# Kernel optimization log

Measured on AMD Instinct MI355X. Metric: run time of the kernel, lower is better.

Reference implementation:

```python
import jax, jax.numpy as jnp
import numpy as np

D_MODEL, N_HEADS, RANK = 1024, 16, 32
HEAD_DIM = D_MODEL // N_HEADS
B, S = 4, 2048


def setup_inputs() -> dict:
    key = jax.random.key(0)
    ks = jax.random.split(key, 8)
    inp = {
        "x": jax.random.normal(ks[0], (B, S, D_MODEL), dtype=jnp.float32),
        "mask": jnp.ones((B, S), dtype=jnp.int32),
        "qkv_u": jax.random.normal(ks[1], (D_MODEL, RANK), jnp.float32) / D_MODEL ** 0.5,
        "qkv_v": jax.random.normal(ks[2], (RANK, 3 * D_MODEL), jnp.float32) / RANK ** 0.5,
        "qkv_b": jnp.zeros((3 * D_MODEL,), jnp.float32),
        "u_attn": jax.random.normal(ks[3], (N_HEADS, HEAD_DIM, RANK), jnp.float32) / HEAD_DIM ** 0.5,
        "v_attn": jax.random.normal(ks[4], (N_HEADS, RANK, HEAD_DIM), jnp.float32) / RANK ** 0.5,
        "out_u": jax.random.normal(ks[5], (D_MODEL, RANK), jnp.float32) / D_MODEL ** 0.5,
        "out_v": jax.random.normal(ks[6], (RANK, D_MODEL), jnp.float32) / RANK ** 0.5,
        "out_b": jnp.zeros((D_MODEL,), jnp.float32),
    }
    return inp


def reference(x, mask, qkv_u, qkv_v, qkv_b, u_attn, v_attn, out_u, out_v, out_b):
    bs, seq_len, d_model = x.shape
    n_heads, head_dim, rank = u_attn.shape
    scale = 1.0 / jnp.sqrt(jnp.float32(rank))

    # Low-rank QKV projection: [B,S,3D]
    qkv = (x @ qkv_u) @ qkv_v + qkv_b
    q, k, v = jnp.split(qkv, 3, axis=-1)

    def to_heads(t):  # [B,S,D] -> [B,H,S,hd]
        return t.reshape(bs, seq_len, n_heads, head_dim).transpose(0, 2, 1, 3)

    q, k, v = to_heads(q), to_heads(k), to_heads(v)

    # Rank-projected Q/K: [B,H,S,r]
    q_low = jnp.einsum("bhsd,hdr->bhsr", q, u_attn)
    k_low = jnp.einsum("bhtd,hdr->bhtr", k, u_attn)
    scores = jnp.einsum("bhsr,bhtr->bhst", q_low, k_low) * scale

    # mask: [B,S] keys; masked_fill where mask == 0
    scores = jnp.where(mask[:, None, None, :] == 0, jnp.float32(-jnp.inf), scores)
    attn = jax.nn.softmax(scores, axis=-1)  # dropout is identity in eval

    v_low = jnp.einsum("bhtd,hdr->bhtr", v, u_attn)
    context_low = jnp.einsum("bhst,bhtr->bhsr", attn, v_low)
    context = jnp.einsum("bhsr,hrd->bhsd", context_low, v_attn)
    context = context.transpose(0, 2, 1, 3).reshape(bs, seq_len, d_model)

    return (context @ out_u) @ out_v + out_b
```

## Files before the change

### kernel.cpp

```cpp
#include <hip/hip_runtime.h>
#include <hip/hip_bf16.h>

typedef unsigned int u32;
typedef unsigned short u16;
typedef __attribute__((ext_vector_type(8))) __bf16 bf16x8;
typedef __attribute__((ext_vector_type(16))) float f32x16;
typedef __attribute__((ext_vector_type(2))) unsigned int u32x2;

#define QSCALE 0.25505418f
#define MFMA __builtin_amdgcn_mfma_f32_32x32x16_bf16

static __device__ __forceinline__ u16 f2b(float f) {
  __hip_bfloat16 h = __float2bfloat16(f);
  return *reinterpret_cast<u16*>(&h);
}
static __device__ __forceinline__ u32 cvtpk(float lo, float hi) {
  u32 r;
  asm("v_cvt_pk_bf16_f32 %0, %1, %2" : "=v"(r) : "v"(lo), "v"(hi));
  return r;
}

static __device__ __forceinline__ float xhalf_sum(float v) {
#if __has_builtin(__builtin_amdgcn_permlane32_swap)
  u32 a = __float_as_uint(v);
  u32x2 r = __builtin_amdgcn_permlane32_swap(a, a, false, false);
  return __uint_as_float(r[0]) + __uint_as_float(r[1]);
#else
  return v + __shfl_xor(v, 32);
#endif
}

static __device__ __forceinline__ int tau(int p) {
  int g = p >> 2;
  int gk = (g & 4) | ((g & 1) << 1) | ((g >> 1) & 1);
  return (gk << 2) | (p & 3);
}

__global__ __launch_bounds__(256) void k_prep(const float* __restrict__ qkv_v,
                                              const float* __restrict__ qkv_b,
                                              const float* __restrict__ u_attn,
                                              const float* __restrict__ v_attn,
                                              const float* __restrict__ out_u,
                                              const float* __restrict__ qkv_u,
                                              const float* __restrict__ out_v,
                                              u16* __restrict__ WQT, u16* __restrict__ WKT,
                                              u16* __restrict__ WVT, float* __restrict__ BQKV,
                                              u16* __restrict__ WOT, u16* __restrict__ UT,
                                              u16* __restrict__ OVT) {
  int blk = blockIdx.x;
  int tid = threadIdx.x;
  if (blk < 16) {
    int h = blk;
    int r = tid & 31, g = tid >> 5;
    for (int rp = g; rp < 32; rp += 8) {
      float aq = 0.f, ak = 0.f, av = 0.f;
      for (int d = 0; d < 64; ++d) {
        float u = u_attn[(h * 64 + d) * 32 + r];
        aq += qkv_v[rp * 3072 + h * 64 + d] * u;
        ak += qkv_v[rp * 3072 + 1024 + h * 64 + d] * u;
        av += qkv_v[rp * 3072 + 2048 + h * 64 + d] * u;
      }
      WQT[(h * 32 + r) * 32 + rp] = f2b(aq);
      WKT[(h * 32 + r) * 32 + rp] = f2b(ak);
      WVT[(h * 32 + r) * 32 + rp] = f2b(av);
    }
    for (int rr = g; rr < 32; rr += 8) {
      float a = 0.f;
      for (int d = 0; d < 64; ++d)
        a += v_attn[(h * 32 + rr) * 64 + d] * out_u[(h * 64 + d) * 32 + r];
      WOT[r * 512 + h * 32 + rr] = f2b(a);
    }
    if (tid < 32) {
      float aq = 0.f, ak = 0.f, av = 0.f;
      for (int d = 0; d < 64; ++d) {
        float u = u_attn[(h * 64 + d) * 32 + r];
        aq += qkv_b[h * 64 + d] * u;
        ak += qkv_b[1024 + h * 64 + d] * u;
        av += qkv_b[2048 + h * 64 + d] * u;
      }
      BQKV[h * 32 + r] = aq;
      BQKV[512 + h * 32 + r] = ak;
      BQKV[1024 + h * 32 + r] = av;
    }
  } else if (blk < 24) {
    int kb = (blk - 16) * 128;
    for (int i = tid; i < 4096; i += 256) {
      int r = i >> 7, kl = i & 127;
      UT[r * 1024 + kb + kl] = f2b(qkv_u[(kb + kl) * 32 + r]);
    }
  } else {
    int db = (blk - 24) * 128;
    for (int i = tid; i < 4096; i += 256) {
      int dl = i >> 5, r = i & 31;
      OVT[(db + dl) * 32 + r] = f2b(out_v[r * 1024 + db + dl]);
    }
  }
}

__global__ __launch_bounds__(512) void k_proj(const float* __restrict__ x,
                                              const u16* __restrict__ UT,
                                              u16* __restrict__ T) {
  __shared__ float red[8][32][33];
  int tid = threadIdx.x;
  int w = tid >> 6, l = tid & 63, lo = l & 31, hi = l >> 5;
  int m0 = blockIdx.x * 32;
  const float* xp = x + (size_t)(m0 + lo) * 1024 + w * 128 + hi * 8;
  const u16* up = UT + lo * 1024 + w * 128 + hi * 8;
  f32x16 acc = {};
  for (int s = 0; s < 8; ++s) {
    float4 x0 = *(const float4*)(xp);
    float4 x1 = *(const float4*)(xp + 4);
    xp += 16;
    union { bf16x8 v; u32 u[4]; } af;
    af.u[0] = cvtpk(x0.x, x0.y);
    af.u[1] = cvtpk(x0.z, x0.w);
    af.u[2] = cvtpk(x1.x, x1.y);
    af.u[3] = cvtpk(x1.z, x1.w);
    bf16x8 bf = *(const bf16x8*)(up);
    up += 16;
    acc = MFMA(af.v, bf, acc, 0, 0, 0);
  }
#pragma unroll
  for (int i = 0; i < 16; ++i)
    red[w][(i & 3) + 8 * (i >> 2) + 4 * hi][lo] = acc[i];
  __syncthreads();
  int m = tid >> 4, c = (tid & 15) * 2;
  float v0 = 0.f, v1 = 0.f;
#pragma unroll
  for (int ww = 0; ww < 8; ++ww) {
    v0 += red[ww][m][c + 0];
    v1 += red[ww][m][c + 1];
  }
  *(u32*)(T + (size_t)(m0 + m) * 32 + c) = cvtpk(v0, v1);
}

__global__ __launch_bounds__(256) void k_lowproj(const u16* __restrict__ T,
                                                 const u16* __restrict__ WQT,
                                                 const u16* __restrict__ WKT,
                                                 const u16* __restrict__ WVT,
                                                 const float* __restrict__ BQKV,
                                                 u16* __restrict__ QL, u16* __restrict__ KF,
                                                 u16* __restrict__ VF) {
  __shared__ float vtf[32][132];
  int tid = threadIdx.x;
  int w = tid >> 6, l = tid & 63, lo = l & 31, hi = l >> 5;
  int blk = blockIdx.x;
  int bh = blk >> 4, sb = (blk & 15) * 128;
  int b = bh >> 4, h = bh & 15;
  int s0 = sb + w * 32;

  const u16* wq = WQT + (h * 32 + lo) * 32 + hi * 8;
  const u16* wk = WKT + (h * 32 + lo) * 32 + hi * 8;
  const u16* wv = WVT + (h * 32 + lo) * 32 + hi * 8;
  bf16x8 aq0 = *(const bf16x8*)(wq), aq1 = *(const bf16x8*)(wq + 16);
  bf16x8 ak0 = *(const bf16x8*)(wk), ak1 = *(const bf16x8*)(wk + 16);
  bf16x8 av0 = *(const bf16x8*)(wv), av1 = *(const bf16x8*)(wv + 16);

  const u16* tp = T + (size_t)(b * 2048 + s0 + lo) * 32 + hi * 8;
  bf16x8 tb0 = *(const bf16x8*)(tp), tb1 = *(const bf16x8*)(tp + 16);

  f32x16 cq = {}, ck = {}, cv = {};
  cq = MFMA(aq0, tb0, cq, 0, 0, 0);
  cq = MFMA(aq1, tb1, cq, 0, 0, 0);
  ck = MFMA(ak0, tb0, ck, 0, 0, 0);
  ck = MFMA(ak1, tb1, ck, 0, 0, 0);
  cv = MFMA(av0, tb0, cv, 0, 0, 0);
  cv = MFMA(av1, tb1, cv, 0, 0, 0);

  size_t sg = (size_t)bh * 2048 + s0 + lo;
  size_t tbase = (size_t)bh * 65536 + (size_t)((sb >> 5) + w) * 1024;
  int slp = w * 32 + tau(lo);
#pragma unroll
  for (int g2 = 0; g2 < 4; ++g2) {
    float4 bq4 = *(const float4*)(BQKV + h * 32 + g2 * 8 + 4 * hi);
    float4 bk4 = *(const float4*)(BQKV + 512 + h * 32 + g2 * 8 + 4 * hi);
    float4 bv4 = *(const float4*)(BQKV + 1024 + h * 32 + g2 * 8 + 4 * hi);
    float q0 = (cq[4 * g2 + 0] + bq4.x) * QSCALE;
    float q1 = (cq[4 * g2 + 1] + bq4.y) * QSCALE;
    float q2 = (cq[4 * g2 + 2] + bq4.z) * QSCALE;
    float q3 = (cq[4 * g2 + 3] + bq4.w) * QSCALE;
    uint2 qo; qo.x = cvtpk(q0, q1); qo.y = cvtpk(q2, q3);
    *(uint2*)(QL + sg * 32 + g2 * 8 + 4 * hi) = qo;
    uint2 ko;
    ko.x = cvtpk(ck[4 * g2 + 0] + bk4.x, ck[4 * g2 + 1] + bk4.y);
    ko.y = cvtpk(ck[4 * g2 + 2] + bk4.z, ck[4 * g2 + 3] + bk4.w);
    *(uint2*)(KF + tbase + (g2 >> 1) * 512 + (g2 & 1) * 256 + lo * 8 + 4 * hi) = ko;
    int rbase = g2 * 8 + 4 * hi;
    vtf[rbase + 0][slp] = cv[4 * g2 + 0] + bv4.x;
    vtf[rbase + 1][slp] = cv[4 * g2 + 1] + bv4.y;
    vtf[rbase + 2][slp] = cv[4 * g2 + 2] + bv4.z;
    vtf[rbase + 3][slp] = cv[4 * g2 + 3] + bv4.w;
  }
  __syncthreads();
  for (int u = tid; u < 512; u += 256) {
    int r = u >> 4, su = (u & 15) * 8;
    const float* src = &vtf[r][su];
    uint4 o;
    o.x = cvtpk(src[0], src[1]);
    o.y = cvtpk(src[2], src[3]);
    o.z = cvtpk(src[4], src[5]);
    o.w = cvtpk(src[6], src[7]);
    int c = su & 31, tloc = su >> 5;
    *(uint4*)(VF + (size_t)bh * 65536 + (size_t)((sb >> 5) + tloc) * 1024 +
              (c >> 4) * 512 + ((c >> 3) & 1) * 256 + r * 8) = o;
  }
}

__global__ __launch_bounds__(256) void k_attn(const u16* __restrict__ QL,
                                              const u16* __restrict__ KF,
                                              const u16* __restrict__ VF,
                                              const int* __restrict__ mask,
                                              u16* __restrict__ CTX) {
  __shared__ float pacc[2][64][17];
  __shared__ float pl[2][64];
  __shared__ u32 cls[64][17];
  int tid = threadIdx.x;
  int wave = tid >> 6, l = tid & 63, lo = l & 31, hi = l >> 5;
  int blk = blockIdx.x;
  int xcd = blk & 7, slot = blk >> 3;
  int bh = xcd * 8 + (slot >> 5);
  int qpair = slot & 31;
  int qi = wave & 1;
  int khalf = wave >> 1;
  int qt = qpair * 2 + qi;
  int b = bh >> 4, h = bh & 15;

  const int* mk = mask + b * 2048;

  int q = qt * 32 + lo;
  const u16* qp = QL + (size_t)bh * 65536 + q * 32 + hi * 8;
  bf16x8 qb0 = *(const bf16x8*)(qp);
  bf16x8 qb1 = *(const bf16x8*)(qp + 16);

  size_t fbase = (size_t)bh * 65536 + (size_t)khalf * 32768 + l * 8;
  const u16* kp = KF + fbase;
  const u16* vp = VF + fbase;

  f32x16 acc = {};
  float l_run = 0.f;

  int mall = 1;
  for (int i = l; i < 2048; i += 64) mall &= (mk[i] != 0) ? 1 : 0;

  if (__all(mall)) {
#pragma unroll 1
    for (int kt = 0; kt < 32; ++kt) {
      bf16x8 ka0 = *(const bf16x8*)(kp);
      bf16x8 ka1 = *(const bf16x8*)(kp + 512);
      kp += 1024;
      f32x16 sc = {};
      sc = MFMA(ka0, qb0, sc, 0, 0, 0);
      sc = MFMA(ka1, qb1, sc, 0, 0, 0);
      bf16x8 va0 = *(const bf16x8*)(vp);
      bf16x8 va1 = *(const bf16x8*)(vp + 512);
      vp += 1024;
      union { bf16x8 v; u32 u[4]; } fa;
      float a0 = __builtin_amdgcn_exp2f(sc[0]);
      float a1 = __builtin_amdgcn_exp2f(sc[1]);
      float a2 = __builtin_amdgcn_exp2f(sc[2]);
      float a3 = __builtin_amdgcn_exp2f(sc[3]);
      fa.u[0] = cvtpk(a0, a1);
      fa.u[1] = cvtpk(a2, a3);
      float t0 = (a0 + a1) + (a2 + a3);
      a0 = __builtin_amdgcn_exp2f(sc[4]);
      a1 = __builtin_amdgcn_exp2f(sc[5]);
      a2 = __builtin_amdgcn_exp2f(sc[6]);
      a3 = __builtin_amdgcn_exp2f(sc[7]);
      fa.u[2] = cvtpk(a0, a1);
      fa.u[3] = cvtpk(a2, a3);
      float t1 = (a0 + a1) + (a2 + a3);
      acc = MFMA(va0, fa.v, acc, 0, 0, 0);
      union { bf16x8 v; u32 u[4]; } fc;
      a0 = __builtin_amdgcn_exp2f(sc[8]);
      a1 = __builtin_amdgcn_exp2f(sc[9]);
      a2 = __builtin_amdgcn_exp2f(sc[10]);
      a3 = __builtin_amdgcn_exp2f(sc[11]);
      fc.u[0] = cvtpk(a0, a1);
      fc.u[1] = cvtpk(a2, a3);
      float t2 = (a0 + a1) + (a2 + a3);
      a0 = __builtin_amdgcn_exp2f(sc[12]);
      a1 = __builtin_amdgcn_exp2f(sc[13]);
      a2 = __builtin_amdgcn_exp2f(sc[14]);
      a3 = __builtin_amdgcn_exp2f(sc[15]);
      fc.u[2] = cvtpk(a0, a1);
      fc.u[3] = cvtpk(a2, a3);
      float t3 = (a0 + a1) + (a2 + a3);
      acc = MFMA(va1, fc.v, acc, 0, 0, 0);
      l_run += (t0 + t1) + (t2 + t3);
    }
  } else {
    const int* mp = mk + khalf * 1024 + lo;
#pragma unroll 1
    for (int kt = 0; kt < 32; ++kt) {
      unsigned long long bm = __ballot(mp[0] != 0);
      mp += 32;
      bf16x8 ka0 = *(const bf16x8*)(kp);
      bf16x8 ka1 = *(const bf16x8*)(kp + 512);
      kp += 1024;
      f32x16 sc = {};
      sc = MFMA(ka0, qb0, sc, 0, 0, 0);
      sc = MFMA(ka1, qb1, sc, 0, 0, 0);
      u32 km = (u32)bm;
#pragma unroll
      for (int i = 0; i < 16; ++i) {
        int key = (i & 3) + 8 * (i >> 2) + 4 * hi;
        if (!((km >> key) & 1)) sc[i] = -3.0e38f;
      }
      bf16x8 va0 = *(const bf16x8*)(vp);
      bf16x8 va1 = *(const bf16x8*)(vp + 512);
      vp += 1024;
      union { bf16x8 v; u32 u[4]; } fa;
      float a0 = __builtin_amdgcn_exp2f(sc[0]);
      float a1 = __builtin_amdgcn_exp2f(sc[1]);
      float a2 = __builtin_amdgcn_exp2f(sc[2]);
      float a3 = __builtin_amdgcn_exp2f(sc[3]);
      fa.u[0] = cvtpk(a0, a1);
      fa.u[1] = cvtpk(a2, a3);
      float t0 = (a0 + a1) + (a2 + a3);
      a0 = __builtin_amdgcn_exp2f(sc[4]);
      a1 = __builtin_amdgcn_exp2f(sc[5]);
      a2 = __builtin_amdgcn_exp2f(sc[6]);
      a3 = __builtin_amdgcn_exp2f(sc[7]);
      fa.u[2] = cvtpk(a0, a1);
      fa.u[3] = cvtpk(a2, a3);
      float t1 = (a0 + a1) + (a2 + a3);
      acc = MFMA(va0, fa.v, acc, 0, 0, 0);
      union { bf16x8 v; u32 u[4]; } fc;
      a0 = __builtin_amdgcn_exp2f(sc[8]);
      a1 = __builtin_amdgcn_exp2f(sc[9]);
      a2 = __builtin_amdgcn_exp2f(sc[10]);
      a3 = __builtin_amdgcn_exp2f(sc[11]);
      fc.u[0] = cvtpk(a0, a1);
      fc.u[1] = cvtpk(a2, a3);
      float t2 = (a0 + a1) + (a2 + a3);
      a0 = __builtin_amdgcn_exp2f(sc[12]);
      a1 = __builtin_amdgcn_exp2f(sc[13]);
      a2 = __builtin_amdgcn_exp2f(sc[14]);
      a3 = __builtin_amdgcn_exp2f(sc[15]);
      fc.u[2] = cvtpk(a0, a1);
      fc.u[3] = cvtpk(a2, a3);
      float t3 = (a0 + a1) + (a2 + a3);
      acc = MFMA(va1, fc.v, acc, 0, 0, 0);
      l_run += (t0 + t1) + (t2 + t3);
    }
  }

  if (khalf) {
#pragma unroll
    for (int i = 0; i < 16; ++i) pacc[qi][l][i] = acc[i];
    pl[qi][l] = l_run;
  }
  __syncthreads();
  if (!khalf) {
#pragma unroll
    for (int i = 0; i < 16; ++i) acc[i] += pacc[qi][l][i];
    l_run += pl[qi][l];
    l_run = xhalf_sum(l_run);
    float inv = 1.0f / l_run;
    int qloc = qi * 32 + lo;
#pragma unroll
    for (int g2 = 0; g2 < 4; ++g2) {
      cls[qloc][g2 * 4 + 2 * hi] = cvtpk(acc[4 * g2 + 0] * inv, acc[4 * g2 + 1] * inv);
      cls[qloc][g2 * 4 + 2 * hi + 1] = cvtpk(acc[4 * g2 + 2] * inv, acc[4 * g2 + 3] * inv);
    }
  }
  __syncthreads();
  int s_loc = tid >> 2, quad = tid & 3;
  int srow = qpair * 64 + s_loc;
  const u32* src = &cls[s_loc][quad * 4];
  uint4 v0;
  v0.x = src[0]; v0.y = src[1]; v0.z = src[2]; v0.w = src[3];
  u16* dst = CTX + (((size_t)(b * 2048 + srow)) * 16 + h) * 32 + quad * 8;
  *(uint4*)(dst) = v0;
}

__global__ __launch_bounds__(512) void k_epi1(const u16* __restrict__ CTX,
                                              const u16* __restrict__ WOT,
                                              u16* __restrict__ YL) {
  __shared__ float red[8][32][33];
  int tid = threadIdx.x;
  int w = tid >> 6, l = tid & 63, lo = l & 31, hi = l >> 5;
  int s0 = blockIdx.x * 32;
  const u16* cp = CTX + (size_t)(s0 + lo) * 512 + w * 64 + hi * 8;
  const u16* wp = WOT + lo * 512 + w * 64 + hi * 8;
  f32x16 acc = {};
  for (int st = 0; st < 4; ++st) {
    bf16x8 a = *(const bf16x8*)(cp);
    bf16x8 bb = *(const bf16x8*)(wp);
    cp += 16;
    wp += 16;
    acc = MFMA(a, bb, acc, 0, 0, 0);
  }
#pragma unroll
  for (int i = 0; i < 16; ++i)
    red[w][(i & 3) + 8 * (i >> 2) + 4 * hi][lo] = acc[i];
  __syncthreads();
  int m = tid >> 4, c = (tid & 15) * 2;
  float v0 = 0.f, v1 = 0.f;
#pragma unroll
  for (int ww = 0; ww < 8; ++ww) {
    v0 += red[ww][m][c + 0];
    v1 += red[ww][m][c + 1];
  }
  *(u32*)(YL + (size_t)(s0 + m) * 32 + c) = cvtpk(v0, v1);
}

__global__ __launch_bounds__(256) void k_epi2(const u16* __restrict__ YL,
                                              const u16* __restrict__ OVT,
                                              const float* __restrict__ out_b,
                                              float* __restrict__ out) {
  __shared__ float ol[32][133];
  int tid = threadIdx.x;
  int w = tid >> 6, l = tid & 63, lo = l & 31, hi = l >> 5;
  int blk = blockIdx.x;
  int s0 = (blk >> 3) * 32;
  int d0 = (blk & 7) * 128;
  int dw = d0 + w * 32;
  const u16* ap = OVT + (size_t)(dw + lo) * 32 + hi * 8;
  bf16x8 a0 = *(const bf16x8*)(ap), a1 = *(const bf16x8*)(ap + 16);
  const u16* bp = YL + (size_t)(s0 + lo) * 32 + hi * 8;
  bf16x8 b0 = *(const bf16x8*)(bp), b1 = *(const bf16x8*)(bp + 16);
  f32x16 acc = {};
  acc = MFMA(a0, b0, acc, 0, 0, 0);
  acc = MFMA(a1, b1, acc, 0, 0, 0);
#pragma unroll
  for (int i = 0; i < 16; ++i)
    ol[lo][w * 32 + (i & 3) + 8 * (i >> 2) + 4 * hi] = acc[i];
  __syncthreads();
  for (int u = tid; u < 1024; u += 256) {
    int s = u >> 5, c = (u & 31) * 4;
    float4 ob = *(const float4*)(out_b + d0 + c);
    float4 o;
    o.x = ol[s][c + 0] + ob.x;
    o.y = ol[s][c + 1] + ob.y;
    o.z = ol[s][c + 2] + ob.z;
    o.w = ol[s][c + 3] + ob.w;
    *(float4*)(out + (size_t)(s0 + s) * 1024 + d0 + c) = o;
  }
}

extern "C" void kernel_launch(void* const* d_in, const int* in_sizes, int n_in,
                              void* d_out, int out_size, void* d_ws, size_t ws_size,
                              hipStream_t stream) {
  const float* x = (const float*)d_in[0];
  const int* mask = (const int*)d_in[1];
  const float* qkv_u = (const float*)d_in[2];
  const float* qkv_v = (const float*)d_in[3];
  const float* qkv_b = (const float*)d_in[4];
  const float* u_attn = (const float*)d_in[5];
  const float* v_attn = (const float*)d_in[6];
  const float* out_u = (const float*)d_in[7];
  const float* out_v = (const float*)d_in[8];
  const float* out_b = (const float*)d_in[9];
  float* out = (float*)d_out;

  char* w = (char*)d_ws;
  u16* WQT = (u16*)(w + 0);
  u16* WKT = (u16*)(w + (32 << 10));
  u16* WVT = (u16*)(w + (64 << 10));
  float* BQ = (float*)(w + (96 << 10));
  u16* WOT = (u16*)(w + (104 << 10));
  u16* UT = (u16*)(w + (136 << 10));
  u16* OVT = (u16*)(w + (200 << 10));
  u16* T = (u16*)(w + (1 << 20));
  u16* QL = (u16*)(w + (2 << 20));
  u16* KF = (u16*)(w + (10 << 20));
  u16* VF = (u16*)(w + (18 << 20));
  u16* CTX = (u16*)(w + (26 << 20));
  u16* YL = (u16*)(w + (34 << 20));

  k_prep<<<32, 256, 0, stream>>>(qkv_v, qkv_b, u_attn, v_attn, out_u, qkv_u, out_v,
                                 WQT, WKT, WVT, BQ, WOT, UT, OVT);
  k_proj<<<256, 512, 0, stream>>>(x, UT, T);
  k_lowproj<<<1024, 256, 0, stream>>>(T, WQT, WKT, WVT, BQ, QL, KF, VF);
  k_attn<<<2048, 256, 0, stream>>>(QL, KF, VF, mask, CTX);
  k_epi1<<<256, 512, 0, stream>>>(CTX, WOT, YL);
  k_epi2<<<2048, 256, 0, stream>>>(YL, OVT, out_b, out);
}
```

Before: 131.3 us.

## Store intermediates in MFMA fragment-major layout and stage x through LDS

Result: faster. 115.1 us (-12.3%).

```diff
diff --git a/kernel.cpp b/kernel.cpp
--- a/kernel.cpp
+++ b/kernel.cpp
@@ -9,6 +9,7 @@
 
 #define QSCALE 0.25505418f
 #define MFMA __builtin_amdgcn_mfma_f32_32x32x16_bf16
+
 
 static __device__ __forceinline__ u16 f2b(float f) {
   __hip_bfloat16 h = __float2bfloat16(f);
@@ -36,6 +37,10 @@
   return (gk << 2) | (p & 3);
 }
 
+static __device__ __forceinline__ int fmoff(int row, int col) {
+  return (col >> 4) * 512 + (((col >> 3) & 1) * 32 + (row & 31)) * 8 + (col & 7);
+}
+
 __global__ __launch_bounds__(256) void k_prep(const float* __restrict__ qkv_v,
                                               const float* __restrict__ qkv_b,
                                               const float* __restrict__ u_attn,
@@ -43,10 +48,10 @@
                                               const float* __restrict__ out_u,
                                               const float* __restrict__ qkv_u,
                                               const float* __restrict__ out_v,
-                                              u16* __restrict__ WQT, u16* __restrict__ WKT,
-                                              u16* __restrict__ WVT, float* __restrict__ BQKV,
-                                              u16* __restrict__ WOT, u16* __restrict__ UT,
-                                              u16* __restrict__ OVT) {
+                                              u16* __restrict__ WQF, u16* __restrict__ WKF,
+                                              u16* __restrict__ WVF, float* __restrict__ BQKV,
+                                              u16* __restrict__ WOTF, u16* __restrict__ UTF,
+                                              u16* __restrict__ OVF) {
   int blk = blockIdx.x;
   int tid = threadIdx.x;
   if (blk < 16) {
@@ -60,15 +65,16 @@
         ak += qkv_v[rp * 3072 + 1024 + h * 64 + d] * u;
         av += qkv_v[rp * 3072 + 2048 + h * 64 + d] * u;
       }
-      WQT[(h * 32 + r) * 32 + rp] = f2b(aq);
-      WKT[(h * 32 + r) * 32 + rp] = f2b(ak);
-      WVT[(h * 32 + r) * 32 + rp] = f2b(av);
+      int o = h * 1024 + fmoff(r, rp);
+      WQF[o] = f2b(aq);
+      WKF[o] = f2b(ak);
+      WVF[o] = f2b(av);
     }
     for (int rr = g; rr < 32; rr += 8) {
       float a = 0.f;
       for (int d = 0; d < 64; ++d)
         a += v_attn[(h * 32 + rr) * 64 + d] * out_u[(h * 64 + d) * 32 + r];
-      WOT[r * 512 + h * 32 + rr] = f2b(a);
+      WOTF[fmoff(r, h * 32 + rr)] = f2b(a);
     }
     if (tid < 32) {
       float aq = 0.f, ak = 0.f, av = 0.f;
@@ -86,39 +92,52 @@
     int kb = (blk - 16) * 128;
     for (int i = tid; i < 4096; i += 256) {
       int r = i >> 7, kl = i & 127;
-      UT[r * 1024 + kb + kl] = f2b(qkv_u[(kb + kl) * 32 + r]);
+      int k = kb + kl;
+      UTF[fmoff(r, k)] = f2b(qkv_u[k * 32 + r]);
     }
   } else {
     int db = (blk - 24) * 128;
     for (int i = tid; i < 4096; i += 256) {
       int dl = i >> 5, r = i & 31;
-      OVT[(db + dl) * 32 + r] = f2b(out_v[r * 1024 + db + dl]);
+      int d = db + dl;
+      OVF[(d >> 5) * 1024 + fmoff(d, r)] = f2b(out_v[r * 1024 + d]);
     }
   }
 }
 
 __global__ __launch_bounds__(512) void k_proj(const float* __restrict__ x,
-                                              const u16* __restrict__ UT,
-                                              u16* __restrict__ T) {
+                                              const u16* __restrict__ UTF,
+                                              u16* __restrict__ TF) {
+  __shared__ float xl[32][129];
   __shared__ float red[8][32][33];
   int tid = threadIdx.x;
   int w = tid >> 6, l = tid & 63, lo = l & 31, hi = l >> 5;
   int m0 = blockIdx.x * 32;
-  const float* xp = x + (size_t)(m0 + lo) * 1024 + w * 128 + hi * 8;
-  const u16* up = UT + lo * 1024 + w * 128 + hi * 8;
+  int srow = tid >> 4, scol = (tid & 15) * 8;
+  const float* xp = x + (size_t)(m0 + srow) * 1024 + scol;
   f32x16 acc = {};
-  for (int s = 0; s < 8; ++s) {
+  for (int ch = 0; ch < 8; ++ch) {
     float4 x0 = *(const float4*)(xp);
     float4 x1 = *(const float4*)(xp + 4);
-    xp += 16;
+    xp += 128;
+    xl[srow][scol + 0] = x0.x;
+    xl[srow][scol + 1] = x0.y;
+    xl[srow][scol + 2] = x0.z;
+    xl[srow][scol + 3] = x0.w;
+    xl[srow][scol + 4] = x1.x;
+    xl[srow][scol + 5] = x1.y;
+    xl[srow][scol + 6] = x1.z;
+    xl[srow][scol + 7] = x1.w;
+    __syncthreads();
+    const float* src = &xl[lo][w * 16 + hi * 8];
     union { bf16x8 v; u32 u[4]; } af;
-    af.u[0] = cvtpk(x0.x, x0.y);
-    af.u[1] = cvtpk(x0.z, x0.w);
-    af.u[2] = cvtpk(x1.x, x1.y);
-    af.u[3] = cvtpk(x1.z, x1.w);
-    bf16x8 bf = *(const bf16x8*)(up);
-    up += 16;
+    af.u[0] = cvtpk(src[0], src[1]);
+    af.u[1] = cvtpk(src[2], src[3]);
+    af.u[2] = cvtpk(src[4], src[5]);
+    af.u[3] = cvtpk(src[6], src[7]);
+    bf16x8 bf = *(const bf16x8*)(UTF + (ch * 8 + w) * 512 + l * 8);
     acc = MFMA(af.v, bf, acc, 0, 0, 0);
+    __syncthreads();
   }
 #pragma unroll
   for (int i = 0; i < 16; ++i)
@@ -131,15 +150,15 @@
     v0 += red[ww][m][c + 0];
     v1 += red[ww][m][c + 1];
   }
-  *(u32*)(T + (size_t)(m0 + m) * 32 + c) = cvtpk(v0, v1);
-}
-
-__global__ __launch_bounds__(256) void k_lowproj(const u16* __restrict__ T,
-                                                 const u16* __restrict__ WQT,
-                                                 const u16* __restrict__ WKT,
-                                                 const u16* __restrict__ WVT,
+  *(u32*)(TF + (size_t)blockIdx.x * 1024 + fmoff(m, c)) = cvtpk(v0, v1);
+}
+
+__global__ __launch_bounds__(256) void k_lowproj(const u16* __restrict__ TF,
+                                                 const u16* __restrict__ WQF,
+                                                 const u16* __restrict__ WKF,
+                                                 const u16* __restrict__ WVF,
                                                  const float* __restrict__ BQKV,
-                                                 u16* __restrict__ QL, u16* __restrict__ KF,
+                                                 u16* __restrict__ QLF, u16* __restrict__ KF,
                                                  u16* __restrict__ VF) {
   __shared__ float vtf[32][132];
   int tid = threadIdx.x;
@@ -147,17 +166,17 @@
   int blk = blockIdx.x;
   int bh = blk >> 4, sb = (blk & 15) * 128;
   int b = bh >> 4, h = bh & 15;
-  int s0 = sb + w * 32;
-
-  const u16* wq = WQT + (h * 32 + lo) * 32 + hi * 8;
-  const u16* wk = WKT + (h * 32 + lo) * 32 + hi * 8;
-  const u16* wv = WVT + (h * 32 + lo) * 32 + hi * 8;
-  bf16x8 aq0 = *(const bf16x8*)(wq), aq1 = *(const bf16x8*)(wq + 16);
-  bf16x8 ak0 = *(const bf16x8*)(wk), ak1 = *(const bf16x8*)(wk + 16);
-  bf16x8 av0 = *(const bf16x8*)(wv), av1 = *(const bf16x8*)(wv + 16);
-
-  const u16* tp = T + (size_t)(b * 2048 + s0 + lo) * 32 + hi * 8;
-  bf16x8 tb0 = *(const bf16x8*)(tp), tb1 = *(const bf16x8*)(tp + 16);
+  int qt = (sb >> 5) + w;
+
+  const u16* wq = WQF + h * 1024 + l * 8;
+  const u16* wk = WKF + h * 1024 + l * 8;
+  const u16* wv = WVF + h * 1024 + l * 8;
+  bf16x8 aq0 = *(const bf16x8*)(wq), aq1 = *(const bf16x8*)(wq + 512);
+  bf16x8 ak0 = *(const bf16x8*)(wk), ak1 = *(const bf16x8*)(wk + 512);
+  bf16x8 av0 = *(const bf16x8*)(wv), av1 = *(const bf16x8*)(wv + 512);
+
+  const u16* tp = TF + (size_t)(b * 64 + qt) * 1024 + l * 8;
+  bf16x8 tb0 = *(const bf16x8*)(tp), tb1 = *(const bf16x8*)(tp + 512);
 
   f32x16 cq = {}, ck = {}, cv = {};
   cq = MFMA(aq0, tb0, cq, 0, 0, 0);
@@ -167,8 +186,8 @@
   cv = MFMA(av0, tb0, cv, 0, 0, 0);
   cv = MFMA(av1, tb1, cv, 0, 0, 0);
 
-  size_t sg = (size_t)bh * 2048 + s0 + lo;
-  size_t tbase = (size_t)bh * 65536 + (size_t)((sb >> 5) + w) * 1024;
+  size_t qbase = (size_t)bh * 65536 + (size_t)qt * 1024;
+  size_t tbase = (size_t)bh * 65536 + (size_t)qt * 1024;
   int slp = w * 32 + tau(lo);
 #pragma unroll
   for (int g2 = 0; g2 < 4; ++g2) {
@@ -180,7 +199,7 @@
     float q2 = (cq[4 * g2 + 2] + bq4.z) * QSCALE;
     float q3 = (cq[4 * g2 + 3] + bq4.w) * QSCALE;
     uint2 qo; qo.x = cvtpk(q0, q1); qo.y = cvtpk(q2, q3);
-    *(uint2*)(QL + sg * 32 + g2 * 8 + 4 * hi) = qo;
+    *(uint2*)(QLF + qbase + (g2 >> 1) * 512 + ((g2 & 1) * 32 + lo) * 8 + 4 * hi) = qo;
     uint2 ko;
     ko.x = cvtpk(ck[4 * g2 + 0] + bk4.x, ck[4 * g2 + 1] + bk4.y);
     ko.y = cvtpk(ck[4 * g2 + 2] + bk4.z, ck[4 * g2 + 3] + bk4.w);
@@ -206,11 +225,11 @@
   }
 }
 
-__global__ __launch_bounds__(256) void k_attn(const u16* __restrict__ QL,
+__global__ __launch_bounds__(256) void k_attn(const u16* __restrict__ QLF,
                                               const u16* __restrict__ KF,
                                               const u16* __restrict__ VF,
                                               const int* __restrict__ mask,
-                                              u16* __restrict__ CTX) {
+                                              u16* __restrict__ CTX2) {
   __shared__ float pacc[2][64][17];
   __shared__ float pl[2][64];
   __shared__ u32 cls[64][17];
@@ -227,10 +246,9 @@
 
   const int* mk = mask + b * 2048;
 
-  int q = qt * 32 + lo;
-  const u16* qp = QL + (size_t)bh * 65536 + q * 32 + hi * 8;
+  const u16* qp = QLF + (size_t)bh * 65536 + (size_t)qt * 1024 + l * 8;
   bf16x8 qb0 = *(const bf16x8*)(qp);
-  bf16x8 qb1 = *(const bf16x8*)(qp + 16);
+  bf16x8 qb1 = *(const bf16x8*)(qp + 512);
 
   size_t fbase = (size_t)bh * 65536 + (size_t)khalf * 32768 + l * 8;
   const u16* kp = KF + fbase;
@@ -365,30 +383,29 @@
     }
   }
   __syncthreads();
-  int s_loc = tid >> 2, quad = tid & 3;
-  int srow = qpair * 64 + s_loc;
-  const u32* src = &cls[s_loc][quad * 4];
+  int st2 = tid >> 7, kcl = (tid >> 6) & 1, lw = tid & 63;
+  const u32* src = &cls[st2 * 32 + (lw & 31)][kcl * 8 + (lw >> 5) * 4];
   uint4 v0;
   v0.x = src[0]; v0.y = src[1]; v0.z = src[2]; v0.w = src[3];
-  u16* dst = CTX + (((size_t)(b * 2048 + srow)) * 16 + h) * 32 + quad * 8;
-  *(uint4*)(dst) = v0;
-}
-
-__global__ __launch_bounds__(512) void k_epi1(const u16* __restrict__ CTX,
-                                              const u16* __restrict__ WOT,
-                                              u16* __restrict__ YL) {
+  *(uint4*)(CTX2 + (size_t)(b * 64 + qpair * 2 + st2) * 16384 +
+            (2 * h + kcl) * 512 + lw * 8) = v0;
+}
+
+__global__ __launch_bounds__(512) void k_epi1(const u16* __restrict__ CTX2,
+                                              const u16* __restrict__ WOTF,
+                                              u16* __restrict__ YLF) {
   __shared__ float red[8][32][33];
   int tid = threadIdx.x;
   int w = tid >> 6, l = tid & 63, lo = l & 31, hi = l >> 5;
-  int s0 = blockIdx.x * 32;
-  const u16* cp = CTX + (size_t)(s0 + lo) * 512 + w * 64 + hi * 8;
-  const u16* wp = WOT + lo * 512 + w * 64 + hi * 8;
+  int stile = blockIdx.x;
+  const u16* cp = CTX2 + (size_t)stile * 16384 + (4 * w) * 512 + l * 8;
+  const u16* wp = WOTF + (4 * w) * 512 + l * 8;
   f32x16 acc = {};
   for (int st = 0; st < 4; ++st) {
     bf16x8 a = *(const bf16x8*)(cp);
     bf16x8 bb = *(const bf16x8*)(wp);
-    cp += 16;
-    wp += 16;
+    cp += 512;
+    wp += 512;
     acc = MFMA(a, bb, acc, 0, 0, 0);
   }
 #pragma unroll
@@ -402,24 +419,25 @@
     v0 += red[ww][m][c + 0];
     v1 += red[ww][m][c + 1];
   }
-  *(u32*)(YL + (size_t)(s0 + m) * 32 + c) = cvtpk(v0, v1);
-}
-
-__global__ __launch_bounds__(256) void k_epi2(const u16* __restrict__ YL,
-                                              const u16* __restrict__ OVT,
+  *(u32*)(YLF + (size_t)stile * 1024 + fmoff(m, c)) = cvtpk(v0, v1);
+}
+
+__global__ __launch_bounds__(256) void k_epi2(const u16* __restrict__ YLF,
+                                              const u16* __restrict__ OVF,
                                               const float* __restrict__ out_b,
                                               float* __restrict__ out) {
   __shared__ float ol[32][133];
   int tid = threadIdx.x;
   int w = tid >> 6, l = tid & 63, lo = l & 31, hi = l >> 5;
   int blk = blockIdx.x;
-  int s0 = (blk >> 3) * 32;
+  int stile = blk >> 3;
+  int s0 = stile * 32;
   int d0 = (blk & 7) * 128;
-  int dw = d0 + w * 32;
-  const u16* ap = OVT + (size_t)(dw + lo) * 32 + hi * 8;
-  bf16x8 a0 = *(const bf16x8*)(ap), a1 = *(const bf16x8*)(ap + 16);
-  const u16* bp = YL + (size_t)(s0 + lo) * 32 + hi * 8;
-  bf16x8 b0 = *(const bf16x8*)(bp), b1 = *(const bf16x8*)(bp + 16);
+  int dtile = (blk & 7) * 4 + w;
+  const u16* ap = OVF + (size_t)dtile * 1024 + l * 8;
+  bf16x8 a0 = *(const bf16x8*)(ap), a1 = *(const bf16x8*)(ap + 512);
+  const u16* bp = YLF + (size_t)stile * 1024 + l * 8;
+  bf16x8 b0 = *(const bf16x8*)(bp), b1 = *(const bf16x8*)(bp + 512);
   f32x16 acc = {};
   acc = MFMA(a0, b0, acc, 0, 0, 0);
   acc = MFMA(a1, b1, acc, 0, 0, 0);
@@ -455,25 +473,25 @@
   float* out = (float*)d_out;
 
   char* w = (char*)d_ws;
-  u16* WQT = (u16*)(w + 0);
-  u16* WKT = (u16*)(w + (32 << 10));
-  u16* WVT = (u16*)(w + (64 << 10));
+  u16* WQF = (u16*)(w + 0);
+  u16* WKF = (u16*)(w + (32 << 10));
+  u16* WVF = (u16*)(w + (64 << 10));
   float* BQ = (float*)(w + (96 << 10));
-  u16* WOT = (u16*)(w + (104 << 10));
-  u16* UT = (u16*)(w + (136 << 10));
-  u16* OVT = (u16*)(w + (200 << 10));
-  u16* T = (u16*)(w + (1 << 20));
-  u16* QL = (u16*)(w + (2 << 20));
+  u16* WOTF = (u16*)(w + (104 << 10));
+  u16* UTF = (u16*)(w + (136 << 10));
+  u16* OVF = (u16*)(w + (200 << 10));
+  u16* TF = (u16*)(w + (1 << 20));
+  u16* QLF = (u16*)(w + (2 << 20));
   u16* KF = (u16*)(w + (10 << 20));
   u16* VF = (u16*)(w + (18 << 20));
-  u16* CTX = (u16*)(w + (26 << 20));
-  u16* YL = (u16*)(w + (34 << 20));
+  u16* CTX2 = (u16*)(w + (26 << 20));
+  u16* YLF = (u16*)(w + (34 << 20));
 
   k_prep<<<32, 256, 0, stream>>>(qkv_v, qkv_b, u_attn, v_attn, out_u, qkv_u, out_v,
-                                 WQT, WKT, WVT, BQ, WOT, UT, OVT);
-  k_proj<<<256, 512, 0, stream>>>(x, UT, T);
-  k_lowproj<<<1024, 256, 0, stream>>>(T, WQT, WKT, WVT, BQ, QL, KF, VF);
-  k_attn<<<2048, 256, 0, stream>>>(QL, KF, VF, mask, CTX);
-  k_epi1<<<256, 512, 0, stream>>>(CTX, WOT, YL);
-  k_epi2<<<2048, 256, 0, stream>>>(YL, OVT, out_b, out);
-}
+                                 WQF, WKF, WVF, BQ, WOTF, UTF, OVF);
+  k_proj<<<256, 512, 0, stream>>>(x, UTF, TF);
+  k_lowproj<<<1024, 256, 0, stream>>>(TF, WQF, WKF, WVF, BQ, QLF, KF, VF);
+  k_attn<<<2048, 256, 0, stream>>>(QLF, KF, VF, mask, CTX2);
+  k_epi1<<<256, 512, 0, stream>>>(CTX2, WOTF, YLF);
+  k_epi2<<<2048, 256, 0, stream>>>(YLF, OVF, out_b, out);
+}
```
